# Performance work log

Hardware: AMD Instinct MI355X
Metric: run time of the kernel (lower is better)

Reference implementation:

```python
import jax, jax.numpy as jnp
import numpy as np

D = 1024      # model_dim
H = 16        # num_heads
DH = D // H   # depth per head
F = 4096      # ffn_dim
B, L = 4, 2048
LN_EPS = 1e-5


def layer_norm(x, g, b):
    mu = jnp.mean(x, axis=-1, keepdims=True)
    var = jnp.var(x, axis=-1, keepdims=True)
    return (x - mu) * jax.lax.rsqrt(var + LN_EPS) * g + b


def setup_inputs() -> dict:
    key = jax.random.key(0)
    ks = jax.random.split(key, 12)
    s = 0.02
    return {
        "inputs": jax.random.normal(ks[0], (B, L, D), jnp.float32),
        "Wq": jax.random.normal(ks[1], (D, D), jnp.float32) * s,
        "Wk": jax.random.normal(ks[2], (D, D), jnp.float32) * s,
        "Wv": jax.random.normal(ks[3], (D, D), jnp.float32) * s,
        "Wo": jax.random.normal(ks[4], (D, D), jnp.float32) * s,
        "W1": jax.random.normal(ks[5], (F, D), jnp.float32) * s,
        "b1": jnp.zeros((F,), jnp.float32),
        "W2": jax.random.normal(ks[6], (D, F), jnp.float32) * s,
        "b2": jnp.zeros((D,), jnp.float32),
        "ln_g": jnp.ones((D,), jnp.float32),
        "ln_b": jnp.zeros((D,), jnp.float32),
    }


def reference(inputs, Wq, Wk, Wv, Wo, W1, b1, W2, b2, ln_g, ln_b):
    # --- MultiHeadAttention (faithful to source, incl. the bug where
    # ScaledDotProductAttention returns v, not attention @ v) ---
    scale = DH ** -0.5
    q = (inputs @ Wq.T) * scale            # [B,L,D], scaled before head split
    k = inputs @ Wk.T                      # [B,L,D]
    v = inputs @ Wv.T                      # [B,L,D]
    # only the LAST head's attention scores survive the python loop
    qH = q[..., (H - 1) * DH:]             # [B,L,DH]
    kH = k[..., (H - 1) * DH:]             # [B,L,DH]
    attn = jax.nn.softmax(jnp.einsum('bqd,bkd->bqk', qH, kH), axis=-1) / H
    # combine_heads(split_heads(v)) == v, so context = Wo applied to v
    context = v @ Wo.T                     # [B,L,D]; dropout(p=0) is identity

    # --- PositionalWiseFeedForward: conv1d(kernel=1) == pointwise linear ---
    h = jax.nn.relu(context @ W1.T + b1)   # [B,L,F]
    ffn = h @ W2.T + b2                    # [B,L,D]
    out = layer_norm(context + ffn, ln_g, ln_b)
    return out, attn
```

## Files before the change

### kernel.cpp

```cpp
#include <hip/hip_runtime.h>
#include <hip/hip_bf16.h>
#include <stdint.h>

#define D_ 1024
#define H_ 16
#define DH_ 64
#define F_ 4096
#define B_ 4
#define L_ 2048
#define MTOK 8192

typedef __attribute__((ext_vector_type(8))) short bf16x8;
typedef __attribute__((ext_vector_type(4))) float f32x4;

__device__ __forceinline__ short f2bf(float f) {
  uint32_t u = __float_as_uint(f);
  uint32_t r = (u + 0x7FFFu + ((u >> 16) & 1u)) >> 16;
  return (short)(uint16_t)r;
}
__device__ __forceinline__ float bf2f(short s) {
  return __uint_as_float(((uint32_t)(uint16_t)s) << 16);
}

__device__ __forceinline__ void gload_lds16(const short* g, short* l) {
  __builtin_amdgcn_global_load_lds(
      (const __attribute__((address_space(1))) void*)g,
      (__attribute__((address_space(3))) void*)l,
      16, 0, 0);
}

__global__ void __launch_bounds__(256) convert_bf16(
    const float* __restrict__ src, short* __restrict__ dst, long n, float scale) {
  long i = ((long)blockIdx.x * 256 + threadIdx.x) * 4;
  long stride = (long)gridDim.x * 1024;
  for (; i < n; i += stride) {
    float4 f = *(const float4*)(src + i);
    short4 o;
    o.x = f2bf(f.x * scale);
    o.y = f2bf(f.y * scale);
    o.z = f2bf(f.z * scale);
    o.w = f2bf(f.w * scale);
    *(short4*)(dst + i) = o;
  }
}

__global__ void __launch_bounds__(256) convert_weights(
    const float* __restrict__ Wq, const float* __restrict__ Wk,
    const float* __restrict__ Wv, const float* __restrict__ Wo,
    const float* __restrict__ W1, const float* __restrict__ W2,
    short* __restrict__ wqk, short* __restrict__ wv, short* __restrict__ wo,
    short* __restrict__ w1, short* __restrict__ w2) {
  long i = ((long)blockIdx.x * 256 + threadIdx.x) * 4;
  const float* src; short* dst; long off; float scale = 1.0f;
  if (i < 65536L)            { src = Wq + 960L * 1024; dst = wqk;        off = i;            scale = 0.125f; }
  else if (i < 131072L)      { src = Wk + 960L * 1024; dst = wqk + 65536; off = i - 65536L;  }
  else if (i < 1179648L)     { src = Wv; dst = wv; off = i - 131072L;   }
  else if (i < 2228224L)     { src = Wo; dst = wo; off = i - 1179648L;  }
  else if (i < 6422528L)     { src = W1; dst = w1; off = i - 2228224L;  }
  else                       { src = W2; dst = w2; off = i - 6422528L;  }
  float4 f = *(const float4*)(src + off);
  short4 o4;
  o4.x = f2bf(f.x * scale); o4.y = f2bf(f.y * scale);
  o4.z = f2bf(f.z * scale); o4.w = f2bf(f.w * scale);
  *(short4*)(dst + off) = o4;
}

__global__ void __launch_bounds__(256) transpose_bf16_1k(
    const short* __restrict__ src, short* __restrict__ dst) {
  __shared__ short t[64][65];
  const int bx = blockIdx.x, by = blockIdx.y;
  const int lr = threadIdx.x >> 4;
  const int lc = (threadIdx.x & 15) * 4;
#pragma unroll
  for (int rr = 0; rr < 4; rr++) {
    int r = lr * 4 + rr;
    short4 v = *(const short4*)&src[(long)(by * 64 + r) * 1024 + bx * 64 + lc];
    t[r][lc] = v.x; t[r][lc + 1] = v.y; t[r][lc + 2] = v.z; t[r][lc + 3] = v.w;
  }
  __syncthreads();
#pragma unroll
  for (int rr = 0; rr < 4; rr++) {
    int r = lr * 4 + rr;
    short4 v;
    v.x = t[lc + 0][r]; v.y = t[lc + 1][r];
    v.z = t[lc + 2][r]; v.w = t[lc + 3][r];
    *(short4*)&dst[(long)(bx * 64 + r) * 1024 + by * 64 + lc] = v;
  }
}

#define FENCE asm volatile("" ::: "memory")
#define BARX  do { FENCE; __builtin_amdgcn_s_barrier(); FENCE; } while (0)
#define PRIO1 __builtin_amdgcn_s_setprio(1)
#define PRIO0 __builtin_amdgcn_s_setprio(0)

#define RD_A(mh_, par_) do {                                                  \
  const short* bp = lds + (par_) * BUF + wm * 4096;                           \
  _Pragma("unroll")                                                           \
  for (int m2 = 0; m2 < 2; m2++) {                                            \
    const int r = ((mh_) * 2 + m2) * 16 + l15;                                \
    _Pragma("unroll")                                                         \
    for (int ks = 0; ks < 2; ks++)                                            \
      aF[mh_][m2][ks] =                                                       \
          *(const bf16x8*)(bp + r * 64 + (((ks * 4 + l4) ^ (r & 7)) << 3));   \
  } } while (0)

#define RD_B(nh_, par_) do {                                                  \
  const short* bp = lds + (par_) * BUF + 8192;                                \
  _Pragma("unroll")                                                           \
  for (int n2 = 0; n2 < 2; n2++) {                                            \
    const int r = wn * 64 + ((nh_) * 2 + n2) * 16 + l15;                      \
    _Pragma("unroll")                                                         \
    for (int ks = 0; ks < 2; ks++)                                            \
      bF[nh_][n2][ks] =                                                       \
          *(const bf16x8*)(bp + r * 64 + (((ks * 4 + l4) ^ (r & 7)) << 3));   \
  } } while (0)

#define QUAD(mh_, nh_) do {                                                   \
  _Pragma("unroll")                                                           \
  for (int ks = 0; ks < 2; ks++)                                              \
    _Pragma("unroll")                                                         \
    for (int m2 = 0; m2 < 2; m2++)                                            \
      _Pragma("unroll")                                                       \
      for (int n2 = 0; n2 < 2; n2++)                                          \
        acc[(mh_) * 2 + m2][(nh_) * 2 + n2] =                                 \
            __builtin_amdgcn_mfma_f32_16x16x32_bf16(                          \
                aF[mh_][m2][ks], bF[nh_][n2][ks],                             \
                acc[(mh_) * 2 + m2][(nh_) * 2 + n2], 0, 0, 0);                \
} while (0)

#define ITER2(g_, par_, SN, SPP, GK) do {                                     \
                    \
  RD_B(0, par_); RD_A(0, par_); RD_B(1, par_);                                \
  if (SN) stA((g_) + 1, 1, (par_) ^ 1);                                       \
  PRIO1; QUAD(0, 0); QUAD(0, 1); PRIO0;                                       \
  BARX;      \
                                                                 \
  RD_A(1, par_);                                                              \
  if (SPP) { stB((g_) + 2, 0, par_); stB((g_) + 2, 1, par_);                  \
             stA((g_) + 2, 0, par_); }                                        \
  PRIO1; QUAD(1, 0); QUAD(1, 1); PRIO0;                                       \
  if (GK == 1) asm volatile("s_waitcnt vmcnt(6)" ::: "memory");               \
  else if (GK == 2) asm volatile("s_waitcnt vmcnt(0)" ::: "memory");          \
  BARX;                          \
} while (0)

template<bool BIAS, bool RELU>
__global__ void __launch_bounds__(256, 2) gemm128(
    const short* __restrict__ A, int lda,
    const short* __restrict__ Bm, int ldb,
    short* __restrict__ C, int ldc,
    const float* __restrict__ bias, int K) {
  constexpr int BUF = 16384;

  __shared__ __align__(16) short lds[2 * BUF];

  const int tid = threadIdx.x;
  const int lane = tid & 63;
  const int wave = tid >> 6;
  const int wm = wave >> 1, wn = wave & 1;
  const int l15 = lane & 15, l4 = lane >> 4;

  const int id = blockIdx.y * gridDim.x + blockIdx.x;
  const int per = (gridDim.x * gridDim.y) >> 3;
  const int swz = (id & 7) * per + (id >> 3);
  const int bn = swz % gridDim.x;
  const int bm = swz / gridDim.x;

  const short* Ab = A + (long)bm * 128 * lda;
  const short* Bb = Bm + (long)bn * 128 * ldb;
  const int NTILE = K >> 6;

  const short* gA[2][2]; short* dA[2][2];
  const short* gB[2][2]; short* dB[2][2];
#pragma unroll
  for (int h = 0; h < 2; h++) {
#pragma unroll
    for (int l = 0; l < 2; l++) {
      int c = l * 256 + tid, r = c >> 3, cg = (c & 7) ^ (r & 7);
      gA[h][l] = Ab + (long)(h * 64 + r) * lda + cg * 8;
      dA[h][l] = lds + h * 4096 + c * 8;
      gB[h][l] = Bb + (long)(h * 64 + r) * ldb + cg * 8;
      dB[h][l] = lds + 8192 + h * 4096 + c * 8;
    }
  }
  auto stA = [&](int t, int h, int par) {
#pragma unroll
    for (int l = 0; l < 2; l++)
      gload_lds16(gA[h][l] + (t << 6), dA[h][l] + par * BUF);
  };
  auto stB = [&](int t, int h, int par) {
#pragma unroll
    for (int l = 0; l < 2; l++)
      gload_lds16(gB[h][l] + (t << 6), dB[h][l] + par * BUF);
  };

  f32x4 acc[4][4];
#pragma unroll
  for (int i = 0; i < 4; i++)
#pragma unroll
    for (int j = 0; j < 4; j++) acc[i][j] = (f32x4){0.f, 0.f, 0.f, 0.f};

  bf16x8 aF[2][2][2];
  bf16x8 bF[2][2][2];

  stA(0, 0, 0); stA(0, 1, 0); stB(0, 0, 0); stB(0, 1, 0);
  stB(1, 0, 1); stB(1, 1, 1); stA(1, 0, 1);
  asm volatile("s_waitcnt vmcnt(6)" ::: "memory");
  BARX;

  for (int g = 0; g + 3 < NTILE; g += 2) {
    ITER2(g, 0, 1, 1, 1);
    ITER2(g + 1, 1, 1, 1, 1);
  }
  ITER2(NTILE - 2, 0, 1, 0, 2);
  ITER2(NTILE - 1, 1, 0, 0, 0);

  const int col0 = bn * 128 + wn * 64;
  const int row0 = bm * 128 + wm * 64;
#pragma unroll
  for (int nt = 0; nt < 4; nt++) {
    const int col = col0 + nt * 16 + l15;
    const float bb = BIAS ? bias[col] : 0.f;
#pragma unroll
    for (int mt = 0; mt < 4; mt++) {
      const int rbase = row0 + mt * 16 + l4 * 4;
#pragma unroll
      for (int r = 0; r < 4; r++) {
        float v = acc[mt][nt][r] + bb;
        if (RELU) v = v > 0.f ? v : 0.f;
        C[(long)(rbase + r) * ldc + col] = f2bf(v);
      }
    }
  }
}

__global__ void __launch_bounds__(256) gemm_bt(
    const short* __restrict__ A, int lda,
    const short* __restrict__ Bm, int ldb,
    short* __restrict__ C, int ldc, int K) {
  const int bn = blockIdx.x;
  const int bm = blockIdx.y;
  const short* Ab = A + (long)bm * 128 * lda;
  const short* Bb = Bm + (long)bn * 128 * ldb;

  __shared__ short lA[128 * 64];
  __shared__ short lB[128 * 64];

  const int tid = threadIdx.x;
  const int lane = tid & 63;
  const int wave = tid >> 6;
  const int wr = wave >> 1, wc = wave & 1;

  f32x4 acc[4][4];
#pragma unroll
  for (int i = 0; i < 4; i++)
#pragma unroll
    for (int j = 0; j < 4; j++) acc[i][j] = (f32x4){0.f, 0.f, 0.f, 0.f};

  for (int k0 = 0; k0 < K; k0 += 64) {
    __syncthreads();
#pragma unroll
    for (int i = 0; i < 4; i++) {
      int c = i * 256 + tid;
      int row = c >> 3;
      int col = (c & 7) * 8;
      gload_lds16(Ab + (long)row * lda + k0 + col, &lA[c * 8]);
      gload_lds16(Bb + (long)row * ldb + k0 + col, &lB[c * 8]);
    }
    __syncthreads();

#pragma unroll
    for (int ks = 0; ks < 2; ks++) {
      bf16x8 af[4], bfr[4];
#pragma unroll
      for (int t = 0; t < 4; t++) {
        af[t]  = *(const bf16x8*)&lA[(wr * 64 + t * 16 + (lane & 15)) * 64 + ks * 32 + (lane >> 4) * 8];
        bfr[t] = *(const bf16x8*)&lB[(wc * 64 + t * 16 + (lane & 15)) * 64 + ks * 32 + (lane >> 4) * 8];
      }
#pragma unroll
      for (int mt = 0; mt < 4; mt++)
#pragma unroll
        for (int nt = 0; nt < 4; nt++)
          acc[mt][nt] = __builtin_amdgcn_mfma_f32_16x16x32_bf16(af[mt], bfr[nt], acc[mt][nt], 0, 0, 0);
    }
  }

  const int col0 = bn * 128 + wc * 64;
  const int row0 = bm * 128 + wr * 64;
#pragma unroll
  for (int mt = 0; mt < 4; mt++) {
#pragma unroll
    for (int nt = 0; nt < 4; nt++) {
      int col = col0 + nt * 16 + (lane & 15);
      int rbase = row0 + mt * 16 + (lane >> 4) * 4;
#pragma unroll
      for (int r = 0; r < 4; r++)
        C[(long)(rbase + r) * ldc + col] = f2bf(acc[mt][nt][r]);
    }
  }
}

__global__ void __launch_bounds__(512) fused_attn(
    const short* __restrict__ qkh, float* __restrict__ attn) {
  const int tid = threadIdx.x;
  const int lane = tid & 63;
  const int wave = tid >> 6;
  const int l15 = lane & 15, l4 = lane >> 4;
  const int b = blockIdx.y;
  const int q0 = blockIdx.x * 16;
  const long base = (long)b * 2048;

  bf16x8 qf[2];
#pragma unroll
  for (int ks = 0; ks < 2; ks++)
    qf[ks] = *(const bf16x8*)&qkh[(base + q0 + l15) * 128 + ks * 32 + l4 * 8];

  const short* kb = qkh + (base + (long)wave * 256) * 128 + 64;

  f32x4 s[16];
#pragma unroll
  for (int kt = 0; kt < 16; kt++) {
    bf16x8 kf0 = *(const bf16x8*)&kb[(kt * 16 + l15) * 128 + l4 * 8];
    bf16x8 kf1 = *(const bf16x8*)&kb[(kt * 16 + l15) * 128 + 32 + l4 * 8];
    f32x4 a = (f32x4){0.f, 0.f, 0.f, 0.f};
    a = __builtin_amdgcn_mfma_f32_16x16x32_bf16(kf0, qf[0], a, 0, 0, 0);
    a = __builtin_amdgcn_mfma_f32_16x16x32_bf16(kf1, qf[1], a, 0, 0, 0);
    s[kt] = a;
  }

  float m = -1e30f;
#pragma unroll
  for (int kt = 0; kt < 16; kt++)
    m = fmaxf(m, fmaxf(fmaxf(s[kt][0], s[kt][1]), fmaxf(s[kt][2], s[kt][3])));
#pragma unroll
  for (int o = 16; o <= 32; o <<= 1) m = fmaxf(m, __shfl_xor(m, o, 64));

  float ss = 0.f;
#pragma unroll
  for (int kt = 0; kt < 16; kt++) {
    f32x4 e;
#pragma unroll
    for (int r = 0; r < 4; r++) e[r] = __expf(s[kt][r] - m);
    s[kt] = e;
    ss += (e[0] + e[1]) + (e[2] + e[3]);
  }
#pragma unroll
  for (int o = 16; o <= 32; o <<= 1) ss += __shfl_xor(ss, o, 64);

  __shared__ float lm[8][16], lsm[8][16];
  if (lane < 16) { lm[wave][l15] = m; lsm[wave][l15] = ss; }
  __syncthreads();
  float M = -1e30f;
#pragma unroll
  for (int w2 = 0; w2 < 8; w2++) M = fmaxf(M, lm[w2][l15]);
  float S = 0.f;
#pragma unroll
  for (int w2 = 0; w2 < 8; w2++) S += lsm[w2][l15] * __expf(lm[w2][l15] - M);
  const float f = __expf(m - M) / (S * 16.0f);

  float* attb = attn + (base + q0 + l15) * 2048 + wave * 256 + l4 * 4;
#pragma unroll
  for (int kt = 0; kt < 16; kt++) {
    f32x4 p;
#pragma unroll
    for (int r = 0; r < 4; r++) p[r] = s[kt][r] * f;
    *(f32x4*)(attb + kt * 16) = p;
  }
}

__device__ __forceinline__ float wave_sum(float v) {
#pragma unroll
  for (int o = 32; o > 0; o >>= 1) v += __shfl_xor(v, o, 64);
  return v;
}

__global__ void __launch_bounds__(256) ln_fuse(
    const short* __restrict__ ctx, const short* __restrict__ ffn,
    const float* __restrict__ g, const float* __restrict__ bta,
    float* __restrict__ out) {
  const int tid = threadIdx.x;
  long base = (long)blockIdx.x * 1024 + tid * 4;
  short4 c4 = *(const short4*)(ctx + base);
  short4 f4 = *(const short4*)(ffn + base);
  float x0 = bf2f(c4.x) + bf2f(f4.x);
  float x1 = bf2f(c4.y) + bf2f(f4.y);
  float x2 = bf2f(c4.z) + bf2f(f4.z);
  float x3 = bf2f(c4.w) + bf2f(f4.w);

  float s = (x0 + x1) + (x2 + x3);
  float q = (x0 * x0 + x1 * x1) + (x2 * x2 + x3 * x3);
  __shared__ float rs[4], rq[4];
  s = wave_sum(s);
  q = wave_sum(q);
  if ((tid & 63) == 0) { rs[tid >> 6] = s; rq[tid >> 6] = q; }
  __syncthreads();
  float S = rs[0] + rs[1] + rs[2] + rs[3];
  float Q = rq[0] + rq[1] + rq[2] + rq[3];
  float mu = S * (1.0f / 1024.0f);
  float var = Q * (1.0f / 1024.0f) - mu * mu;
  float inv = rsqrtf(var + 1e-5f);

  float4 g4 = *(const float4*)(g + tid * 4);
  float4 b4 = *(const float4*)(bta + tid * 4);
  float4 o;
  o.x = (x0 - mu) * inv * g4.x + b4.x;
  o.y = (x1 - mu) * inv * g4.y + b4.y;
  o.z = (x2 - mu) * inv * g4.z + b4.z;
  o.w = (x3 - mu) * inv * g4.w + b4.w;
  *(float4*)(out + base) = o;
}

extern "C" void kernel_launch(void* const* d_in, const int* in_sizes, int n_in,
                              void* d_out, int out_size, void* d_ws, size_t ws_size,
                              hipStream_t stream) {
  const float* inputs = (const float*)d_in[0];
  const float* Wq = (const float*)d_in[1];
  const float* Wk = (const float*)d_in[2];
  const float* Wv = (const float*)d_in[3];
  const float* Wo = (const float*)d_in[4];
  const float* W1 = (const float*)d_in[5];
  const float* b1 = (const float*)d_in[6];
  const float* W2 = (const float*)d_in[7];
  const float* b2 = (const float*)d_in[8];
  const float* ln_g = (const float*)d_in[9];
  const float* ln_b = (const float*)d_in[10];

  char* w = (char*)d_ws;
  short* in_bf = (short*)w;  w += (long)MTOK * D_ * 2;
  short* wqk   = (short*)w;  w += 128L * D_ * 2;
  short* wv    = (short*)w;  w += (long)D_ * D_ * 2;
  short* wo    = (short*)w;  w += (long)D_ * D_ * 2;
  short* w1    = (short*)w;  w += (long)F_ * D_ * 2;
  short* w2    = (short*)w;  w += (long)D_ * F_ * 2;
  short* qkh   = (short*)w;  w += (long)MTOK * 128 * 2;
  short* wvT   = (short*)w;  w += (long)D_ * D_ * 2;
  short* wf    = (short*)w;  w += (long)D_ * D_ * 2;
  short* ctxbf = (short*)w;  w += (long)MTOK * D_ * 2;
  short* hbf   = (short*)w;  w += (long)MTOK * F_ * 2;
  short* ffnbf = (short*)w;  w += (long)MTOK * D_ * 2;

  float* out  = (float*)d_out;
  float* attn = out + (long)MTOK * D_;

  convert_bf16<<<dim3((MTOK * D_) >> 10), 256, 0, stream>>>(
      inputs, in_bf, (long)MTOK * D_, 1.0f);
  convert_weights<<<dim3(10368), 256, 0, stream>>>(
      Wq, Wk, Wv, Wo, W1, W2, wqk, wv, wo, w1, w2);

  transpose_bf16_1k<<<dim3(16, 16), 256, 0, stream>>>(wv, wvT);
  gemm_bt<<<dim3(8, 8), 256, 0, stream>>>(wo, D_, wvT, D_, wf, D_, D_);

  gemm_bt<<<dim3(1, 64), 256, 0, stream>>>(in_bf, D_, wqk, D_, qkh, 128, D_);
  fused_attn<<<dim3(128, 4), 512, 0, stream>>>(qkh, attn);
  gemm128<false, false><<<dim3(8, 64), 256, 0, stream>>>(
      in_bf, D_, wf, D_, ctxbf, D_, nullptr, D_);
  gemm128<true, true><<<dim3(32, 64), 256, 0, stream>>>(
      ctxbf, D_, w1, D_, hbf, F_, b1, D_);
  gemm128<true, false><<<dim3(8, 64), 256, 0, stream>>>(
      hbf, F_, w2, F_, ffnbf, D_, b2, F_);
  ln_fuse<<<dim3(MTOK), 256, 0, stream>>>(ctxbf, ffnbf, ln_g, ln_b, out);
}
```

Measured before the change: 286.3 us.

## Replace GEMM kernels with triple-buffered K32 pipeline and merge conversion launches

Replaces the double-buffered 64-wide K tile GEMM (and the simple gemm_bt) with a single kernel using a three-stage LDS ring of 32-wide K tiles, one barrier per step, and launch bounds allowing three blocks per CU. It also folds the input conversion into the weight conversion kernel to save a launch. The intent is deeper prefetch and higher occupancy to hide global-load latency. It drops the XOR swizzle on LDS reads and doubles barrier count, which risks bank conflicts and more sync overhead.

```diff
diff --git a/kernel.cpp b/kernel.cpp
--- a/kernel.cpp
+++ b/kernel.cpp
@@ -29,35 +29,27 @@
       16, 0, 0);
 }
 
-__global__ void __launch_bounds__(256) convert_bf16(
-    const float* __restrict__ src, short* __restrict__ dst, long n, float scale) {
-  long i = ((long)blockIdx.x * 256 + threadIdx.x) * 4;
-  long stride = (long)gridDim.x * 1024;
-  for (; i < n; i += stride) {
-    float4 f = *(const float4*)(src + i);
-    short4 o;
-    o.x = f2bf(f.x * scale);
-    o.y = f2bf(f.y * scale);
-    o.z = f2bf(f.z * scale);
-    o.w = f2bf(f.w * scale);
-    *(short4*)(dst + i) = o;
-  }
-}
-
-__global__ void __launch_bounds__(256) convert_weights(
+#define FENCE asm volatile("" ::: "memory")
+#define BARX  do { FENCE; __builtin_amdgcn_s_barrier(); FENCE; } while (0)
+#define PRIO1 __builtin_amdgcn_s_setprio(1)
+#define PRIO0 __builtin_amdgcn_s_setprio(0)
+
+__global__ void __launch_bounds__(256) convert_all(
     const float* __restrict__ Wq, const float* __restrict__ Wk,
     const float* __restrict__ Wv, const float* __restrict__ Wo,
     const float* __restrict__ W1, const float* __restrict__ W2,
+    const float* __restrict__ inputs,
     short* __restrict__ wqk, short* __restrict__ wv, short* __restrict__ wo,
-    short* __restrict__ w1, short* __restrict__ w2) {
+    short* __restrict__ w1, short* __restrict__ w2, short* __restrict__ in_bf) {
   long i = ((long)blockIdx.x * 256 + threadIdx.x) * 4;
   const float* src; short* dst; long off; float scale = 1.0f;
-  if (i < 65536L)            { src = Wq + 960L * 1024; dst = wqk;        off = i;            scale = 0.125f; }
-  else if (i < 131072L)      { src = Wk + 960L * 1024; dst = wqk + 65536; off = i - 65536L;  }
-  else if (i < 1179648L)     { src = Wv; dst = wv; off = i - 131072L;   }
-  else if (i < 2228224L)     { src = Wo; dst = wo; off = i - 1179648L;  }
-  else if (i < 6422528L)     { src = W1; dst = w1; off = i - 2228224L;  }
-  else                       { src = W2; dst = w2; off = i - 6422528L;  }
+  if (i < 65536L)        { src = Wq + 960L * 1024; dst = wqk;         off = i;            scale = 0.125f; }
+  else if (i < 131072L)  { src = Wk + 960L * 1024; dst = wqk + 65536; off = i - 65536L;   }
+  else if (i < 1179648L) { src = Wv;     dst = wv;    off = i - 131072L;   }
+  else if (i < 2228224L) { src = Wo;     dst = wo;    off = i - 1179648L;  }
+  else if (i < 6422528L) { src = W1;     dst = w1;    off = i - 2228224L;  }
+  else if (i < 10616832L){ src = W2;     dst = w2;    off = i - 6422528L;  }
+  else                   { src = inputs; dst = in_bf; off = i - 10616832L; }
   float4 f = *(const float4*)(src + off);
   short4 o4;
   o4.x = f2bf(f.x * scale); o4.y = f2bf(f.y * scale);
@@ -88,71 +80,15 @@
   }
 }
 
-#define FENCE asm volatile("" ::: "memory")
-#define BARX  do { FENCE; __builtin_amdgcn_s_barrier(); FENCE; } while (0)
-#define PRIO1 __builtin_amdgcn_s_setprio(1)
-#define PRIO0 __builtin_amdgcn_s_setprio(0)
-
-#define RD_A(mh_, par_) do {                                                  \
-  const short* bp = lds + (par_) * BUF + wm * 4096;                           \
-  _Pragma("unroll")                                                           \
-  for (int m2 = 0; m2 < 2; m2++) {                                            \
-    const int r = ((mh_) * 2 + m2) * 16 + l15;                                \
-    _Pragma("unroll")                                                         \
-    for (int ks = 0; ks < 2; ks++)                                            \
-      aF[mh_][m2][ks] =                                                       \
-          *(const bf16x8*)(bp + r * 64 + (((ks * 4 + l4) ^ (r & 7)) << 3));   \
-  } } while (0)
-
-#define RD_B(nh_, par_) do {                                                  \
-  const short* bp = lds + (par_) * BUF + 8192;                                \
-  _Pragma("unroll")                                                           \
-  for (int n2 = 0; n2 < 2; n2++) {                                            \
-    const int r = wn * 64 + ((nh_) * 2 + n2) * 16 + l15;                      \
-    _Pragma("unroll")                                                         \
-    for (int ks = 0; ks < 2; ks++)                                            \
-      bF[nh_][n2][ks] =                                                       \
-          *(const bf16x8*)(bp + r * 64 + (((ks * 4 + l4) ^ (r & 7)) << 3));   \
-  } } while (0)
-
-#define QUAD(mh_, nh_) do {                                                   \
-  _Pragma("unroll")                                                           \
-  for (int ks = 0; ks < 2; ks++)                                              \
-    _Pragma("unroll")                                                         \
-    for (int m2 = 0; m2 < 2; m2++)                                            \
-      _Pragma("unroll")                                                       \
-      for (int n2 = 0; n2 < 2; n2++)                                          \
-        acc[(mh_) * 2 + m2][(nh_) * 2 + n2] =                                 \
-            __builtin_amdgcn_mfma_f32_16x16x32_bf16(                          \
-                aF[mh_][m2][ks], bF[nh_][n2][ks],                             \
-                acc[(mh_) * 2 + m2][(nh_) * 2 + n2], 0, 0, 0);                \
-} while (0)
-
-#define ITER2(g_, par_, SN, SPP, GK) do {                                     \
-                    \
-  RD_B(0, par_); RD_A(0, par_); RD_B(1, par_);                                \
-  if (SN) stA((g_) + 1, 1, (par_) ^ 1);                                       \
-  PRIO1; QUAD(0, 0); QUAD(0, 1); PRIO0;                                       \
-  BARX;      \
-                                                                 \
-  RD_A(1, par_);                                                              \
-  if (SPP) { stB((g_) + 2, 0, par_); stB((g_) + 2, 1, par_);                  \
-             stA((g_) + 2, 0, par_); }                                        \
-  PRIO1; QUAD(1, 0); QUAD(1, 1); PRIO0;                                       \
-  if (GK == 1) asm volatile("s_waitcnt vmcnt(6)" ::: "memory");               \
-  else if (GK == 2) asm volatile("s_waitcnt vmcnt(0)" ::: "memory");          \
-  BARX;                          \
-} while (0)
-
 template<bool BIAS, bool RELU>
-__global__ void __launch_bounds__(256, 2) gemm128(
+__global__ void __launch_bounds__(256, 3) gemm_r3(
     const short* __restrict__ A, int lda,
     const short* __restrict__ Bm, int ldb,
     short* __restrict__ C, int ldc,
     const float* __restrict__ bias, int K) {
-  constexpr int BUF = 16384;
-
-  __shared__ __align__(16) short lds[2 * BUF];
+  constexpr int ABUF = 4096;
+  constexpr int BUF  = 8192;
+  __shared__ __align__(16) short lds[3 * BUF];
 
   const int tid = threadIdx.x;
   const int lane = tid & 63;
@@ -168,31 +104,33 @@
 
   const short* Ab = A + (long)bm * 128 * lda;
   const short* Bb = Bm + (long)bn * 128 * ldb;
-  const int NTILE = K >> 6;
-
-  const short* gA[2][2]; short* dA[2][2];
-  const short* gB[2][2]; short* dB[2][2];
-#pragma unroll
-  for (int h = 0; h < 2; h++) {
-#pragma unroll
-    for (int l = 0; l < 2; l++) {
-      int c = l * 256 + tid, r = c >> 3, cg = (c & 7) ^ (r & 7);
-      gA[h][l] = Ab + (long)(h * 64 + r) * lda + cg * 8;
-      dA[h][l] = lds + h * 4096 + c * 8;
-      gB[h][l] = Bb + (long)(h * 64 + r) * ldb + cg * 8;
-      dB[h][l] = lds + 8192 + h * 4096 + c * 8;
-    }
-  }
-  auto stA = [&](int t, int h, int par) {
-#pragma unroll
-    for (int l = 0; l < 2; l++)
-      gload_lds16(gA[h][l] + (t << 6), dA[h][l] + par * BUF);
+  const int NTILE = K >> 5;
+
+  const short* gA[2]; const short* gB[2]; int dOf[2];
+#pragma unroll
+  for (int l = 0; l < 2; l++) {
+    int c = l * 256 + tid;
+    int r = c >> 2, kg = c & 3;
+    gA[l] = Ab + (long)r * lda + kg * 8;
+    gB[l] = Bb + (long)r * ldb + kg * 8;
+    dOf[l] = c * 8;
+  }
+  auto stage = [&](int t, int pS) {
+    const int k0 = t << 5;
+#pragma unroll
+    for (int l = 0; l < 2; l++) gload_lds16(gA[l] + k0, lds + pS + dOf[l]);
+#pragma unroll
+    for (int l = 0; l < 2; l++) gload_lds16(gB[l] + k0, lds + pS + ABUF + dOf[l]);
   };
-  auto stB = [&](int t, int h, int par) {
-#pragma unroll
-    for (int l = 0; l < 2; l++)
-      gload_lds16(gB[h][l] + (t << 6), dB[h][l] + par * BUF);
-  };
+
+  int aOf[4], bOf[4];
+#pragma unroll
+  for (int t = 0; t < 4; t++) {
+    int ra = wm * 64 + t * 16 + l15;
+    int rb = wn * 64 + t * 16 + l15;
+    aOf[t] = (ra * 4 + l4) * 8;
+    bOf[t] = ABUF + (rb * 4 + l4) * 8;
+  }
 
   f32x4 acc[4][4];
 #pragma unroll
@@ -200,20 +138,33 @@
 #pragma unroll
     for (int j = 0; j < 4; j++) acc[i][j] = (f32x4){0.f, 0.f, 0.f, 0.f};
 
-  bf16x8 aF[2][2][2];
-  bf16x8 bF[2][2][2];
-
-  stA(0, 0, 0); stA(0, 1, 0); stB(0, 0, 0); stB(0, 1, 0);
-  stB(1, 0, 1); stB(1, 1, 1); stA(1, 0, 1);
-  asm volatile("s_waitcnt vmcnt(6)" ::: "memory");
+  stage(0, 0); stage(1, BUF);
+  asm volatile("s_waitcnt vmcnt(4)" ::: "memory");
   BARX;
 
-  for (int g = 0; g + 3 < NTILE; g += 2) {
-    ITER2(g, 0, 1, 1, 1);
-    ITER2(g + 1, 1, 1, 1, 1);
-  }
-  ITER2(NTILE - 2, 0, 1, 0, 2);
-  ITER2(NTILE - 1, 1, 0, 0, 0);
+  int p0 = 0, p1 = BUF, p2 = 2 * BUF;
+  for (int g = 0; g < NTILE; g++) {
+    bf16x8 aF[4], bF[4];
+#pragma unroll
+    for (int t = 0; t < 4; t++) aF[t] = *(const bf16x8*)(lds + p0 + aOf[t]);
+#pragma unroll
+    for (int t = 0; t < 4; t++) bF[t] = *(const bf16x8*)(lds + p0 + bOf[t]);
+    if (g + 2 < NTILE) stage(g + 2, p2);
+    PRIO1;
+#pragma unroll
+    for (int mt = 0; mt < 4; mt++)
+#pragma unroll
+      for (int nt = 0; nt < 4; nt++)
+        acc[mt][nt] = __builtin_amdgcn_mfma_f32_16x16x32_bf16(
+            aF[mt], bF[nt], acc[mt][nt], 0, 0, 0);
+    PRIO0;
+    if (g + 2 < NTILE)
+      asm volatile("s_waitcnt vmcnt(4)" ::: "memory");
+    else if (g + 1 < NTILE)
+      asm volatile("s_waitcnt vmcnt(0)" ::: "memory");
+    BARX;
+    int tmp = p0; p0 = p1; p1 = p2; p2 = tmp;
+  }
 
   const int col0 = bn * 128 + wn * 64;
   const int row0 = bm * 128 + wm * 64;
@@ -230,72 +181,6 @@
         if (RELU) v = v > 0.f ? v : 0.f;
         C[(long)(rbase + r) * ldc + col] = f2bf(v);
       }
-    }
-  }
-}
-
-__global__ void __launch_bounds__(256) gemm_bt(
-    const short* __restrict__ A, int lda,
-    const short* __restrict__ Bm, int ldb,
-    short* __restrict__ C, int ldc, int K) {
-  const int bn = blockIdx.x;
-  const int bm = blockIdx.y;
-  const short* Ab = A + (long)bm * 128 * lda;
-  const short* Bb = Bm + (long)bn * 128 * ldb;
-
-  __shared__ short lA[128 * 64];
-  __shared__ short lB[128 * 64];
-
-  const int tid = threadIdx.x;
-  const int lane = tid & 63;
-  const int wave = tid >> 6;
-  const int wr = wave >> 1, wc = wave & 1;
-
-  f32x4 acc[4][4];
-#pragma unroll
-  for (int i = 0; i < 4; i++)
-#pragma unroll
-    for (int j = 0; j < 4; j++) acc[i][j] = (f32x4){0.f, 0.f, 0.f, 0.f};
-
-  for (int k0 = 0; k0 < K; k0 += 64) {
-    __syncthreads();
-#pragma unroll
-    for (int i = 0; i < 4; i++) {
-      int c = i * 256 + tid;
-      int row = c >> 3;
-      int col = (c & 7) * 8;
-      gload_lds16(Ab + (long)row * lda + k0 + col, &lA[c * 8]);
-      gload_lds16(Bb + (long)row * ldb + k0 + col, &lB[c * 8]);
-    }
-    __syncthreads();
-
-#pragma unroll
-    for (int ks = 0; ks < 2; ks++) {
-      bf16x8 af[4], bfr[4];
-#pragma unroll
-      for (int t = 0; t < 4; t++) {
-        af[t]  = *(const bf16x8*)&lA[(wr * 64 + t * 16 + (lane & 15)) * 64 + ks * 32 + (lane >> 4) * 8];
-        bfr[t] = *(const bf16x8*)&lB[(wc * 64 + t * 16 + (lane & 15)) * 64 + ks * 32 + (lane >> 4) * 8];
-      }
-#pragma unroll
-      for (int mt = 0; mt < 4; mt++)
-#pragma unroll
-        for (int nt = 0; nt < 4; nt++)
-          acc[mt][nt] = __builtin_amdgcn_mfma_f32_16x16x32_bf16(af[mt], bfr[nt], acc[mt][nt], 0, 0, 0);
-    }
-  }
-
-  const int col0 = bn * 128 + wc * 64;
-  const int row0 = bm * 128 + wr * 64;
-#pragma unroll
-  for (int mt = 0; mt < 4; mt++) {
-#pragma unroll
-    for (int nt = 0; nt < 4; nt++) {
-      int col = col0 + nt * 16 + (lane & 15);
-      int rbase = row0 + mt * 16 + (lane >> 4) * 4;
-#pragma unroll
-      for (int r = 0; r < 4; r++)
-        C[(long)(rbase + r) * ldc + col] = f2bf(acc[mt][nt][r]);
     }
   }
 }
@@ -442,21 +327,21 @@
   float* out  = (float*)d_out;
   float* attn = out + (long)MTOK * D_;
 
-  convert_bf16<<<dim3((MTOK * D_) >> 10), 256, 0, stream>>>(
-      inputs, in_bf, (long)MTOK * D_, 1.0f);
-  convert_weights<<<dim3(10368), 256, 0, stream>>>(
-      Wq, Wk, Wv, Wo, W1, W2, wqk, wv, wo, w1, w2);
+  convert_all<<<dim3(18560), 256, 0, stream>>>(
+      Wq, Wk, Wv, Wo, W1, W2, inputs, wqk, wv, wo, w1, w2, in_bf);
 
   transpose_bf16_1k<<<dim3(16, 16), 256, 0, stream>>>(wv, wvT);
-  gemm_bt<<<dim3(8, 8), 256, 0, stream>>>(wo, D_, wvT, D_, wf, D_, D_);
-
-  gemm_bt<<<dim3(1, 64), 256, 0, stream>>>(in_bf, D_, wqk, D_, qkh, 128, D_);
+  gemm_r3<false, false><<<dim3(8, 8), 256, 0, stream>>>(
+      wo, D_, wvT, D_, wf, D_, nullptr, D_);
+
+  gemm_r3<false, false><<<dim3(1, 64), 256, 0, stream>>>(
+      in_bf, D_, wqk, D_, qkh, 128, nullptr, D_);
   fused_attn<<<dim3(128, 4), 512, 0, stream>>>(qkh, attn);
-  gemm128<false, false><<<dim3(8, 64), 256, 0, stream>>>(
+  gemm_r3<false, false><<<dim3(8, 64), 256, 0, stream>>>(
       in_bf, D_, wf, D_, ctxbf, D_, nullptr, D_);
-  gemm128<true, true><<<dim3(32, 64), 256, 0, stream>>>(
+  gemm_r3<true, true><<<dim3(32, 64), 256, 0, stream>>>(
       ctxbf, D_, w1, D_, hbf, F_, b1, D_);
-  gemm128<true, false><<<dim3(8, 64), 256, 0, stream>>>(
+  gemm_r3<true, false><<<dim3(8, 64), 256, 0, stream>>>(
       hbf, F_, w2, F_, ffnbf, D_, b2, F_);
   ln_fuse<<<dim3(MTOK), 256, 0, stream>>>(ctxbf, ffnbf, ln_g, ln_b, out);
 }
```

Measured after the change: 290.1 us. No clear change (+1.3%).
